# Optimization experiments

Hardware: AMD Instinct MI355X
Metric: run time of the kernel (lower is better)

Reference implementation:

```python
import jax, jax.numpy as jnp
import numpy as np

QMAX = 127.0  # int8 symmetric fake-quant (brevitas-style, per-tensor scale)

def fq(x):
    s = jnp.maximum(jnp.max(jnp.abs(x)), 1e-8) / QMAX
    q = jnp.clip(jnp.round(x / s), -QMAX - 1.0, QMAX) * s
    # straight-through estimator (round_ste), matches brevitas gradient behavior
    return x + jax.lax.stop_gradient(q - x)

def layernorm(x, g, b, eps=1e-5):
    m = x.mean(-1, keepdims=True)
    v = x.var(-1, keepdims=True)
    return (x - m) * jax.lax.rsqrt(v + eps) * g + b

def mamba_dir(u, W_in, conv_w, conv_b, W_xp, W_dt, b_dt, A_log, D_skip, W_out):
    # u: [B, L, D]
    B, L, D = u.shape
    di, K = conv_w.shape
    ds = A_log.shape[-1]
    dtr = W_dt.shape[0]
    xz = u @ W_in                              # [B, L, 2*di]
    xc, z = jnp.split(xz, 2, axis=-1)
    xb = xc.transpose(0, 2, 1)                 # [B, di, L]
    xb = jax.lax.conv_general_dilated(
        xb, conv_w[:, None, :], (1,), [(K - 1, 0)],
        feature_group_count=di,
        dimension_numbers=('NCH', 'OIH', 'NCH')) + conv_b[None, :, None]
    xs = jax.nn.silu(xb.transpose(0, 2, 1))    # [B, L, di]
    proj = xs @ W_xp                           # [B, L, dtr+2*ds]
    dt_in = proj[..., :dtr]
    Bc = proj[..., dtr:dtr + ds]
    Cc = proj[..., dtr + ds:]
    dt = jax.nn.softplus(dt_in @ W_dt + b_dt)  # [B, L, di]
    A = -jnp.exp(A_log)                        # [di, ds]

    def step(h, inp):
        dt_t, B_t, C_t, x_t = inp              # [B,di],[B,ds],[B,ds],[B,di]
        dA = jnp.exp(dt_t[..., None] * A)      # [B, di, ds]
        h = dA * h + (dt_t * x_t)[..., None] * B_t[:, None, :]
        y = jnp.einsum('bds,bs->bd', h, C_t)
        return h, y

    h0 = jnp.zeros((B, di, ds), u.dtype)
    t = lambda a: jnp.moveaxis(a, 1, 0)        # [L, B, ...]
    _, ys = jax.lax.scan(step, h0, (t(dt), t(Bc), t(Cc), t(xs)))
    y = jnp.moveaxis(ys, 0, 1) + xs * D_skip   # [B, L, di]
    y = y * jax.nn.silu(z)
    return y @ W_out                           # [B, L, D]


def setup_inputs() -> dict:
    key = jax.random.key(0)
    ks = jax.random.split(key, 20)
    B, H, W = 32, 16, 4096
    p = 2
    emb = 32
    gh, gw = (H - p) // p + 1, (W - p) // p + 1   # 8, 2048
    D = gh * emb                                   # 256
    di = min(2 * D, 256)                           # 256
    ds, K, nb, nc = 8, 4, 2, 10
    dtr = (D + 15) // 16                           # 16
    f32 = jnp.float32
    n = lambda k, s, sc: jax.random.normal(k, s, f32) * sc
    return {
        'x': jax.random.normal(ks[0], (B, 1, H, W), f32),
        'patch_w': n(ks[1], (emb, 1, p, p), 0.3),
        'patch_b': jnp.zeros((emb,), f32),
        'pos_embed': n(ks[2], (1, gw, D), 0.02),
        'W_in': n(ks[3], (nb, 2, D, 2 * di), D ** -0.5),
        'conv_w': n(ks[4], (nb, 2, di, K), 0.3),
        'conv_b': jnp.zeros((nb, 2, di), f32),
        'W_xp': n(ks[5], (nb, 2, di, dtr + 2 * ds), di ** -0.5),
        'W_dt': n(ks[6], (nb, 2, dtr, di), dtr ** -0.5),
        'b_dt': jnp.full((nb, 2, di), -3.0, f32),
        'A_log': jnp.log(jnp.broadcast_to(jnp.arange(1, ds + 1, dtype=f32), (nb, 2, di, ds))),
        'D_skip': jnp.ones((nb, 2, di), f32),
        'W_out': n(ks[7], (nb, 2, di, D), di ** -0.5),
        'ln_g': jnp.ones((nb, D), f32),
        'ln_b': jnp.zeros((nb, D), f32),
        'cls_w': n(ks[8], (nc, D), D ** -0.5),
        'cls_b': jnp.zeros((nc,), f32),
    }


def reference(x, patch_w, patch_b, pos_embed, W_in, conv_w, conv_b, W_xp, W_dt,
              b_dt, A_log, D_skip, W_out, ln_g, ln_b, cls_w, cls_b):
    x = fq(x)
    # quantized patch embed: conv2d stride=patch, then [B,C,gh,gw] -> [B, gw, gh*C]
    xe = jax.lax.conv_general_dilated(
        x, fq(patch_w), (2, 2), 'VALID',
        dimension_numbers=('NCHW', 'OIHW', 'NCHW')) + patch_b[None, :, None, None]
    B, C, gh, gw = xe.shape
    h = fq(xe.transpose(0, 3, 2, 1).reshape(B, gw, gh * C))
    pos = fq(pos_embed)
    h, pos = fq(h), fq(pos)     # scale_equalizer on both operands
    h = fq(h + pos)
    nb = W_in.shape[0]
    for i in range(nb):
        res = h
        yf = mamba_dir(h, W_in[i, 0], conv_w[i, 0], conv_b[i, 0], W_xp[i, 0],
                       W_dt[i, 0], b_dt[i, 0], A_log[i, 0], D_skip[i, 0], W_out[i, 0])
        yb = jnp.flip(mamba_dir(jnp.flip(h, 1), W_in[i, 1], conv_w[i, 1], conv_b[i, 1],
                                W_xp[i, 1], W_dt[i, 1], b_dt[i, 1], A_log[i, 1],
                                D_skip[i, 1], W_out[i, 1]), 1)
        y = fq(yf + yb)          # bidirectional_strategy='add' + block output quant
        h = fq(layernorm(res + y, ln_g[i], ln_b[i]))
    pooled = fq(h.mean(axis=1))  # AdaptiveAvgPool1d(1) over sequence
    return pooled @ fq(cls_w).T + cls_b
```

## Files before the change

kernel.cpp:

```cpp
#include <hip/hip_runtime.h>


typedef __attribute__((ext_vector_type(8))) short bfrag;
typedef __attribute__((ext_vector_type(4))) float cfrag;

__device__ __forceinline__ float fq_val(float x, float s){
  float q = rintf(x / s);
  q = fminf(fmaxf(q, -128.0f), 127.0f);
  return q * s;
}
__device__ __forceinline__ float g_of(float a){ return fmaxf(a, 1e-8f) / 127.0f; }

__device__ __forceinline__ short f2bf(float f){
  unsigned u = __float_as_uint(f);
  u += 0x7fff + ((u >> 16) & 1);
  return (short)(u >> 16);
}
__device__ __forceinline__ float bf2f(short h){
  return __uint_as_float(((unsigned)(unsigned short)h) << 16);
}

__device__ __forceinline__ void bk_absmax(float v, float* bkt){
  for (int m = 32; m; m >>= 1) v = fmaxf(v, __shfl_xor(v, m));
  __shared__ float wmax[4];
  int lane = threadIdx.x & 63, wid = threadIdx.x >> 6;
  if (lane == 0) wmax[wid] = v;
  __syncthreads();
  if (threadIdx.x == 0){
    float m = fmaxf(fmaxf(wmax[0], wmax[1]), fmaxf(wmax[2], wmax[3]));
    atomicMax((unsigned int*)&bkt[(blockIdx.x & 63) * 16], __float_as_uint(m));
  }
}

__global__ __launch_bounds__(256) void absmax_b(const float* __restrict__ x,
                                                long long n, float* __restrict__ bkt){
  float m = 0.0f;
  for (long long i = (long long)blockIdx.x * 256 + threadIdx.x; i < n;
       i += (long long)gridDim.x * 256)
    m = fmaxf(m, fabsf(x[i]));
  bk_absmax(m, bkt);
}

__global__ __launch_bounds__(64) void combine_kernel(const float* __restrict__ bkt,
                                                     float* __restrict__ slot){
  float v = bkt[(threadIdx.x & 63) * 16];
  for (int m = 32; m; m >>= 1) v = fmaxf(v, __shfl_xor(v, m));
  if (threadIdx.x == 0) slot[0] = v;
}

__global__ __launch_bounds__(64) void chain_kernel(float* __restrict__ sc){
  if (threadIdx.x == 0){
    float s1 = g_of(sc[1]);
    float a1 = fq_val(sc[1], s1);
    sc[2] = s1; sc[3] = g_of(a1);
    float p1 = g_of(sc[4]);
    float a2 = fq_val(sc[4], p1);
    sc[5] = p1; sc[6] = g_of(a2);
  }
}

__global__ __launch_bounds__(256) void fq_small(const float* __restrict__ src,
                                                float* __restrict__ dst, int n){
  __shared__ float red[256];
  __shared__ float sS;
  float m = 0.0f;
  for (int i = threadIdx.x; i < n; i += 256) m = fmaxf(m, fabsf(src[i]));
  red[threadIdx.x] = m; __syncthreads();
  for (int s2 = 128; s2 > 0; s2 >>= 1){
    if (threadIdx.x < s2) red[threadIdx.x] = fmaxf(red[threadIdx.x], red[threadIdx.x + s2]);
    __syncthreads();
  }
  if (threadIdx.x == 0) sS = g_of(red[0]);
  __syncthreads();
  float s = sS;
  for (int i = threadIdx.x; i < n; i += 256) dst[i] = fq_val(src[i], s);
}

__global__ __launch_bounds__(256) void wsplit(const float* __restrict__ src,
                                              short* __restrict__ dh,
                                              short* __restrict__ dl, int N){
  __shared__ float tile[64][65];
  int n0 = blockIdx.x * 64, k0 = blockIdx.y * 64, id = blockIdx.z;
  const float* S = src + (long long)id * 256 * N;
  short* H = dh + (long long)id * N * 256;
  short* L = dl + (long long)id * N * 256;
  int t = threadIdx.x;
#pragma unroll
  for (int i = 0; i < 16; i++){
    int idx = i * 256 + t;
    int kr = idx >> 6, nc = idx & 63;
    tile[kr][nc] = S[(long long)(k0 + kr) * N + n0 + nc];
  }
  __syncthreads();
#pragma unroll
  for (int i = 0; i < 16; i++){
    int idx = i * 256 + t;
    int nr = idx >> 6, kc = idx & 63;
    float f = tile[kc][nr];
    short h = f2bf(f);
    short l = f2bf(f - bf2f(h));
    H[(long long)(n0 + nr) * 256 + k0 + kc] = h;
    L[(long long)(n0 + nr) * 256 + k0 + kc] = l;
  }
}

__global__ __launch_bounds__(256) void patchify_kernel(const float* __restrict__ x,
                                                       const float* __restrict__ pwq,
                                                       const float* __restrict__ pb,
                                                       float* __restrict__ h,
                                                       const float* __restrict__ slot,
                                                       float* __restrict__ bkt){
  int t = blockIdx.x * 256 + threadIdx.x;
  int q = t & 63;
  int l = (t >> 6) & 2047;
  int b = t >> 17;
  int d0 = q * 4;
  int c0 = d0 & 31, g = d0 >> 5;
  float s = g_of(slot[0]);
  const float* xp = x + ((long long)(b * 16 + 2 * g) * 4096 + 2 * l);
  float x0 = fq_val(xp[0], s),    x1 = fq_val(xp[1], s);
  float x2 = fq_val(xp[4096], s), x3 = fq_val(xp[4097], s);
  float4 o; float* op = (float*)&o;
  float mx = 0.0f;
#pragma unroll
  for (int j = 0; j < 4; j++){
    int c = c0 + j;
    float a = pb[c] + x0 * pwq[c * 4] + x1 * pwq[c * 4 + 1]
                    + x2 * pwq[c * 4 + 2] + x3 * pwq[c * 4 + 3];
    op[j] = a; mx = fmaxf(mx, fabsf(a));
  }
  *(float4*)(h + (long long)t * 4) = o;
  bk_absmax(mx, bkt);
}

__global__ __launch_bounds__(256) void addpos_kernel(float* __restrict__ h,
                                                     const float* __restrict__ pos,
                                                     const float* __restrict__ sc,
                                                     float* __restrict__ bkt){
  long long t = (long long)blockIdx.x * 256 + threadIdx.x;
  float s1 = sc[2], s2 = sc[3], p1 = sc[5], p2 = sc[6];
  float4 hv = *(const float4*)(h + t * 4);
  float4 pv = *(const float4*)(pos + ((t * 4) & 524287));
  float* hp = (float*)&hv; float* pp = (float*)&pv;
  float4 o; float* op = (float*)&o;
  float mx = 0.0f;
#pragma unroll
  for (int j = 0; j < 4; j++){
    float v = fq_val(fq_val(hp[j], s1), s2) + fq_val(fq_val(pp[j], p1), p2);
    op[j] = v; mx = fmaxf(mx, fabsf(v));
  }
  *(float4*)(h + t * 4) = o;
  bk_absmax(mx, bkt);
}

__global__ __launch_bounds__(256) void aprep(const float* __restrict__ h,
                                             const float* __restrict__ slot,
                                             short* __restrict__ Aq){
  long long t = (long long)blockIdx.x * 256 + threadIdx.x;
  float sA = g_of(slot[0]);
  float4 v0 = *(const float4*)(h + t * 8);
  float4 v1 = *(const float4*)(h + t * 8 + 4);
  float* vp0 = (float*)&v0; float* vp1 = (float*)&v1;
  bfrag o;
#pragma unroll
  for (int j = 0; j < 4; j++){
    o[j]     = f2bf(fminf(fmaxf(rintf(vp0[j] / sA), -128.0f), 127.0f));
    o[j + 4] = f2bf(fminf(fmaxf(rintf(vp1[j] / sA), -128.0f), 127.0f));
  }
  *(bfrag*)(Aq + t * 8) = o;
}

__global__ __launch_bounds__(256) void gemm_win(const short* __restrict__ Aq,
                                                const short* __restrict__ BhT,
                                                const short* __restrict__ BlT,
                                                float* __restrict__ Cx,
                                                float* __restrict__ Cz,
                                                int flipA,
                                                const float* __restrict__ aslot){
  __shared__ short Ah[128][40];
  __shared__ short Bh[128][40];
  __shared__ short Bl[128][40];
  int t = threadIdx.x;
  int bn = blockIdx.x, bm = blockIdx.y;
  int lane = t & 63, wv = t >> 6;
  int wm = wv & 1, wn = wv >> 1;
  int qd = lane >> 4, l16 = lane & 15;
  float sA = g_of(aslot[0]);

  int r0s = t >> 2, c8s = (t & 3) * 8;
  int r1s = r0s + 64;
  long long am0, am1;
  {
    long long mg0 = (long long)bm * 128 + r0s;
    long long mg1 = (long long)bm * 128 + r1s;
    am0 = flipA ? ((mg0 & ~2047LL) + (2047 - (mg0 & 2047))) : mg0;
    am1 = flipA ? ((mg1 & ~2047LL) + (2047 - (mg1 & 2047))) : mg1;
  }
  const short* Aq0 = Aq + am0 * 256 + c8s;
  const short* Aq1 = Aq + am1 * 256 + c8s;
  const short* Bh0 = BhT + (long long)(bn * 128 + r0s) * 256 + c8s;
  const short* Bh1 = BhT + (long long)(bn * 128 + r1s) * 256 + c8s;
  const short* Bl0 = BlT + (long long)(bn * 128 + r0s) * 256 + c8s;
  const short* Bl1 = BlT + (long long)(bn * 128 + r1s) * 256 + c8s;

  bfrag aR0, aR1, bhR0, bhR1, blR0, blR1;
  aR0 = *(const bfrag*)(Aq0);   aR1 = *(const bfrag*)(Aq1);
  bhR0 = *(const bfrag*)(Bh0);  bhR1 = *(const bfrag*)(Bh1);
  blR0 = *(const bfrag*)(Bl0);  blR1 = *(const bfrag*)(Bl1);

  cfrag acc[4][4];
#pragma unroll
  for (int i = 0; i < 4; i++)
#pragma unroll
    for (int j = 0; j < 4; j++)
      acc[i][j] = (cfrag){0.f, 0.f, 0.f, 0.f};

  for (int k0 = 0; k0 < 256; k0 += 32){
    *(bfrag*)&Ah[r0s][c8s] = aR0;  *(bfrag*)&Ah[r1s][c8s] = aR1;
    *(bfrag*)&Bh[r0s][c8s] = bhR0; *(bfrag*)&Bh[r1s][c8s] = bhR1;
    *(bfrag*)&Bl[r0s][c8s] = blR0; *(bfrag*)&Bl[r1s][c8s] = blR1;
    __syncthreads();
    if (k0 < 224){
      int kn = k0 + 32;
      aR0 = *(const bfrag*)(Aq0 + kn);   aR1 = *(const bfrag*)(Aq1 + kn);
      bhR0 = *(const bfrag*)(Bh0 + kn);  bhR1 = *(const bfrag*)(Bh1 + kn);
      blR0 = *(const bfrag*)(Bl0 + kn);  blR1 = *(const bfrag*)(Bl1 + kn);
    }
    bfrag bh[4], bl[4], a[4];
#pragma unroll
    for (int ni = 0; ni < 4; ni++){
      int nrow = wn * 64 + ni * 16 + l16;
      bh[ni] = *(const bfrag*)&Bh[nrow][qd * 8];
      bl[ni] = *(const bfrag*)&Bl[nrow][qd * 8];
    }
#pragma unroll
    for (int mi = 0; mi < 4; mi++)
      a[mi] = *(const bfrag*)&Ah[wm * 64 + mi * 16 + l16][qd * 8];
#pragma unroll
    for (int mi = 0; mi < 4; mi++)
#pragma unroll
      for (int ni = 0; ni < 4; ni++)
        acc[mi][ni] = __builtin_amdgcn_mfma_f32_16x16x32_bf16(a[mi], bh[ni], acc[mi][ni], 0, 0, 0);
#pragma unroll
    for (int mi = 0; mi < 4; mi++)
#pragma unroll
      for (int ni = 0; ni < 4; ni++)
        acc[mi][ni] = __builtin_amdgcn_mfma_f32_16x16x32_bf16(a[mi], bl[ni], acc[mi][ni], 0, 0, 0);
    __syncthreads();
  }

  float* Co = (bn < 2) ? Cx : Cz;
  int cb = (bn & 1) * 128;
#pragma unroll
  for (int mi = 0; mi < 4; mi++){
#pragma unroll
    for (int ni = 0; ni < 4; ni++){
      int colg = cb + wn * 64 + ni * 16 + l16;
#pragma unroll
      for (int r = 0; r < 4; r++){
        long long mg = (long long)bm * 128 + wm * 64 + mi * 16 + qd * 4 + r;
        Co[mg * 256 + colg] = acc[mi][ni][r] * sA;
      }
    }
  }
}

__global__ __launch_bounds__(256) void gemm_wout(const float* __restrict__ A,
                                                 const short* __restrict__ BhT,
                                                 const short* __restrict__ BlT,
                                                 float* __restrict__ C,
                                                 int flipC, int accum,
                                                 float* __restrict__ bkt){
  __shared__ short Ah[128][40];
  __shared__ short Al[128][40];
  __shared__ short Bh[128][40];
  __shared__ short Bl[128][40];
  int t = threadIdx.x;
  int bn = blockIdx.x, bm = blockIdx.y;
  int lane = t & 63, wv = t >> 6;
  int wm = wv & 1, wn = wv >> 1;
  int qd = lane >> 4, l16 = lane & 15;

  int ra0 = t >> 3, ca0 = (t & 7) * 4;
  const float* Ap0 = A + ((long long)bm * 128 + ra0) * 256 + ca0;
  const float* Ap1 = Ap0 + 32 * 256;
  const float* Ap2 = Ap0 + 64 * 256;
  const float* Ap3 = Ap0 + 96 * 256;
  int rb0 = t >> 2, cb8 = (t & 3) * 8;
  int rb1 = rb0 + 64;
  const short* Bh0 = BhT + (long long)(bn * 128 + rb0) * 256 + cb8;
  const short* Bh1 = BhT + (long long)(bn * 128 + rb1) * 256 + cb8;
  const short* Bl0 = BlT + (long long)(bn * 128 + rb0) * 256 + cb8;
  const short* Bl1 = BlT + (long long)(bn * 128 + rb1) * 256 + cb8;

  uint4 aw0, aw1, aw2, aw3;
  bfrag bhR0, bhR1, blR0, blR1;
  aw0 = *(const uint4*)(Ap0); aw1 = *(const uint4*)(Ap1);
  aw2 = *(const uint4*)(Ap2); aw3 = *(const uint4*)(Ap3);
  bhR0 = *(const bfrag*)(Bh0); bhR1 = *(const bfrag*)(Bh1);
  blR0 = *(const bfrag*)(Bl0); blR1 = *(const bfrag*)(Bl1);

  cfrag acc[4][4];
#pragma unroll
  for (int i = 0; i < 4; i++)
#pragma unroll
    for (int j = 0; j < 4; j++)
      acc[i][j] = (cfrag){0.f, 0.f, 0.f, 0.f};

  for (int k0 = 0; k0 < 256; k0 += 32){
    {
      unsigned* w;
      w = (unsigned*)&aw0;
#pragma unroll
      for (int j = 0; j < 4; j++){ Ah[ra0][ca0+j] = (short)(w[j] & 0xffff); Al[ra0][ca0+j] = (short)(w[j] >> 16); }
      w = (unsigned*)&aw1;
#pragma unroll
      for (int j = 0; j < 4; j++){ Ah[ra0+32][ca0+j] = (short)(w[j] & 0xffff); Al[ra0+32][ca0+j] = (short)(w[j] >> 16); }
      w = (unsigned*)&aw2;
#pragma unroll
      for (int j = 0; j < 4; j++){ Ah[ra0+64][ca0+j] = (short)(w[j] & 0xffff); Al[ra0+64][ca0+j] = (short)(w[j] >> 16); }
      w = (unsigned*)&aw3;
#pragma unroll
      for (int j = 0; j < 4; j++){ Ah[ra0+96][ca0+j] = (short)(w[j] & 0xffff); Al[ra0+96][ca0+j] = (short)(w[j] >> 16); }
      *(bfrag*)&Bh[rb0][cb8] = bhR0; *(bfrag*)&Bh[rb1][cb8] = bhR1;
      *(bfrag*)&Bl[rb0][cb8] = blR0; *(bfrag*)&Bl[rb1][cb8] = blR1;
    }
    __syncthreads();
    if (k0 < 224){
      int kn = k0 + 32;
      aw0 = *(const uint4*)(Ap0 + kn); aw1 = *(const uint4*)(Ap1 + kn);
      aw2 = *(const uint4*)(Ap2 + kn); aw3 = *(const uint4*)(Ap3 + kn);
      bhR0 = *(const bfrag*)(Bh0 + kn); bhR1 = *(const bfrag*)(Bh1 + kn);
      blR0 = *(const bfrag*)(Bl0 + kn); blR1 = *(const bfrag*)(Bl1 + kn);
    }
    bfrag bh[4], bl[4], ah[4], al[4];
#pragma unroll
    for (int ni = 0; ni < 4; ni++){
      int nrow = wn * 64 + ni * 16 + l16;
      bh[ni] = *(const bfrag*)&Bh[nrow][qd * 8];
      bl[ni] = *(const bfrag*)&Bl[nrow][qd * 8];
    }
#pragma unroll
    for (int mi = 0; mi < 4; mi++){
      int mrow = wm * 64 + mi * 16 + l16;
      ah[mi] = *(const bfrag*)&Ah[mrow][qd * 8];
      al[mi] = *(const bfrag*)&Al[mrow][qd * 8];
    }
#pragma unroll
    for (int mi = 0; mi < 4; mi++)
#pragma unroll
      for (int ni = 0; ni < 4; ni++)
        acc[mi][ni] = __builtin_amdgcn_mfma_f32_16x16x32_bf16(ah[mi], bh[ni], acc[mi][ni], 0, 0, 0);
#pragma unroll
    for (int mi = 0; mi < 4; mi++)
#pragma unroll
      for (int ni = 0; ni < 4; ni++)
        acc[mi][ni] = __builtin_amdgcn_mfma_f32_16x16x32_bf16(al[mi], bh[ni], acc[mi][ni], 0, 0, 0);
#pragma unroll
    for (int mi = 0; mi < 4; mi++)
#pragma unroll
      for (int ni = 0; ni < 4; ni++)
        acc[mi][ni] = __builtin_amdgcn_mfma_f32_16x16x32_bf16(ah[mi], bl[ni], acc[mi][ni], 0, 0, 0);
    __syncthreads();
  }

  float mx = 0.0f;
#pragma unroll
  for (int mi = 0; mi < 4; mi++){
#pragma unroll
    for (int ni = 0; ni < 4; ni++){
      int colg = bn * 128 + wn * 64 + ni * 16 + l16;
#pragma unroll
      for (int r = 0; r < 4; r++){
        long long mg = (long long)bm * 128 + wm * 64 + mi * 16 + qd * 4 + r;
        long long mr = flipC ? ((mg & ~2047LL) + (2047 - (mg & 2047))) : mg;
        float* Cp = C + mr * 256 + colg;
        if (accum){
          float nv = *Cp + acc[mi][ni][r];
          *Cp = nv;
          mx = fmaxf(mx, fabsf(nv));
        } else {
          *Cp = acc[mi][ni][r];
        }
      }
    }
  }
  if (bkt) bk_absmax(mx, bkt);
}

__global__ __launch_bounds__(256) void conv_proj(const float* __restrict__ xc,
                                                 const float* __restrict__ cw,
                                                 const float* __restrict__ cb,
                                                 const float* __restrict__ Wxp,
                                                 float* __restrict__ xs,
                                                 float* __restrict__ proj){
  __shared__ float As[8][256];
  long long r0 = (long long)blockIdx.x * 8;
  int l0 = (int)(r0 & 2047);
  int d = threadIdx.x;
  float w0 = cw[d*4], w1 = cw[d*4+1], w2 = cw[d*4+2], w3 = cw[d*4+3];
  float cbd = cb[d];
  const float* base = xc + r0 * 256 + d;
  float vm3 = (l0 >= 3) ? base[-768] : 0.0f;
  float vm2 = (l0 >= 2) ? base[-512] : 0.0f;
  float vm1 = (l0 >= 1) ? base[-256] : 0.0f;
#pragma unroll
  for (int r = 0; r < 8; r++){
    float v0 = base[r * 256];
    float a = cbd + w3 * v0 + w2 * vm1 + w1 * vm2 + w0 * vm3;
    float sv = __fdividef(a, 1.0f + __expf(-a));
    As[r][d] = sv;
    xs[r0 * 256 + r * 256 + d] = sv;
    vm3 = vm2; vm2 = vm1; vm1 = v0;
  }
  __syncthreads();
  int rr = threadIdx.x >> 5, cc = threadIdx.x & 31;
  float acc = 0.0f;
#pragma unroll 8
  for (int k = 0; k < 256; k++) acc = fmaf(As[rr][k], Wxp[k * 32 + cc], acc);
  proj[(r0 + rr) * 32 + cc] = acc;
}

__global__ __launch_bounds__(256) void scan1_kernel(const float* __restrict__ xs,
                                                    const float* __restrict__ proj,
                                                    const float* __restrict__ Wdt,
                                                    const float* __restrict__ bdt,
                                                    const float* __restrict__ A_log,
                                                    float* __restrict__ Pb,
                                                    float* __restrict__ Qb){
  __shared__ float pj[32][32];
  int blk = blockIdx.x;
  int seg = blk & 63, b = blk >> 6;
  int d = threadIdx.x;
  long long rowbase = (long long)b * 2048 + seg * 32;
  {
    const float4* src4 = (const float4*)(proj + rowbase * 32);
    float4* dst4 = (float4*)&pj[0][0];
    if (threadIdx.x < 256) dst4[threadIdx.x] = src4[threadIdx.x];
  }
  __syncthreads();
  float wdt[16];
#pragma unroll
  for (int r = 0; r < 16; r++) wdt[r] = Wdt[r * 256 + d];
  float bd = bdt[d];
  float A[8];
#pragma unroll
  for (int s = 0; s < 8; s++) A[s] = -expf(A_log[d * 8 + s]);
  const float* xp = xs + rowbase * 256 + d;
  float P[8], q[8];
#pragma unroll
  for (int s = 0; s < 8; s++){ P[s] = 1.0f; q[s] = 0.0f; }
  for (int l = 0; l < 32; l++){
    float acc = bd;
#pragma unroll
    for (int r = 0; r < 16; r++) acc = fmaf(pj[l][r], wdt[r], acc);
    float e = __expf(-fabsf(acc));
    float dt = fmaxf(acc, 0.0f) + __logf(1.0f + e);
    float x = xp[(long long)l * 256];
    float dx = dt * x;
#pragma unroll
    for (int s = 0; s < 8; s++){
      float dA = __expf(dt * A[s]);
      P[s] *= dA;
      q[s] = fmaf(dA, q[s], dx * pj[l][16 + s]);
    }
  }
  long long obase = ((long long)blk << 11) + (long long)d * 8;
  *(float4*)(Pb + obase)     = make_float4(P[0], P[1], P[2], P[3]);
  *(float4*)(Pb + obase + 4) = make_float4(P[4], P[5], P[6], P[7]);
  *(float4*)(Qb + obase)     = make_float4(q[0], q[1], q[2], q[3]);
  *(float4*)(Qb + obase + 4) = make_float4(q[4], q[5], q[6], q[7]);
}

__global__ __launch_bounds__(256) void scan2_kernel(float* __restrict__ Pb,
                                                    const float* __restrict__ Qb){
  int t = blockIdx.x * 256 + threadIdx.x;
  int ds_ = t & 2047;
  int b = t >> 11;
  float h = 0.0f;
#pragma unroll
  for (int g = 0; g < 64; g++){
    long long idx = (((long long)b * 64 + g) << 11) + ds_;
    float tp = Pb[idx];
    Pb[idx] = h;
    h = fmaf(tp, h, Qb[idx]);
  }
}

__global__ __launch_bounds__(256) void scan3_kernel(const float* __restrict__ z,
                                                    float* __restrict__ xs,
                                                    const float* __restrict__ proj,
                                                    const float* __restrict__ Wdt,
                                                    const float* __restrict__ bdt,
                                                    const float* __restrict__ A_log,
                                                    const float* __restrict__ Dsk,
                                                    const float* __restrict__ Hs){
  __shared__ float pj[32][32];
  int blk = blockIdx.x;
  int seg = blk & 63, b = blk >> 6;
  int d = threadIdx.x;
  long long rowbase = (long long)b * 2048 + seg * 32;
  {
    const float4* src4 = (const float4*)(proj + rowbase * 32);
    float4* dst4 = (float4*)&pj[0][0];
    if (threadIdx.x < 256) dst4[threadIdx.x] = src4[threadIdx.x];
  }
  __syncthreads();
  float wdt[16];
#pragma unroll
  for (int r = 0; r < 16; r++) wdt[r] = Wdt[r * 256 + d];
  float bd = bdt[d];
  float A[8];
#pragma unroll
  for (int s = 0; s < 8; s++) A[s] = -expf(A_log[d * 8 + s]);
  float Dv = Dsk[d];
  long long hbase = ((long long)blk << 11) + (long long)d * 8;
  float4 h0 = *(const float4*)(Hs + hbase);
  float4 h1 = *(const float4*)(Hs + hbase + 4);
  float h[8] = {h0.x, h0.y, h0.z, h0.w, h1.x, h1.y, h1.z, h1.w};
  float* xp = xs + rowbase * 256 + d;
  const float* zp = z + rowbase * 256 + d;
  for (int l = 0; l < 32; l++){
    float acc = bd;
#pragma unroll
    for (int r = 0; r < 16; r++) acc = fmaf(pj[l][r], wdt[r], acc);
    float e = __expf(-fabsf(acc));
    float dt = fmaxf(acc, 0.0f) + __logf(1.0f + e);
    float x = xp[(long long)l * 256];
    float dx = dt * x;
    float y = 0.0f;
#pragma unroll
    for (int s = 0; s < 8; s++){
      float dA = __expf(dt * A[s]);
      h[s] = fmaf(dA, h[s], dx * pj[l][16 + s]);
      y = fmaf(h[s], pj[l][24 + s], y);
    }
    y = fmaf(x, Dv, y);
    float zv = zp[(long long)l * 256];
    float yg = y * __fdividef(zv, 1.0f + __expf(-zv));
    short hh = f2bf(yg);
    short ll = f2bf(yg - bf2f(hh));
    xp[(long long)l * 256] =
        __uint_as_float(((unsigned)(unsigned short)ll << 16) | (unsigned short)hh);
  }
}

__global__ __launch_bounds__(256) void ln_kernel(const float* __restrict__ hraw,
                                                 const float* __restrict__ hslot,
                                                 float* __restrict__ y,
                                                 const float* __restrict__ yslot,
                                                 const float* __restrict__ g,
                                                 const float* __restrict__ bb,
                                                 float* __restrict__ bkt){
  int wid = threadIdx.x >> 6, lane = threadIdx.x & 63;
  long long row = (long long)blockIdx.x * 4 + wid;
  long long o = row * 256 + lane * 4;
  float sh = g_of(hslot[0]);
  float sy = g_of(yslot[0]);
  float4 hv = *(const float4*)(hraw + o);
  float4 yv = *(const float4*)(y + o);
  float t0 = fq_val(hv.x, sh) + fq_val(yv.x, sy);
  float t1 = fq_val(hv.y, sh) + fq_val(yv.y, sy);
  float t2 = fq_val(hv.z, sh) + fq_val(yv.z, sy);
  float t3 = fq_val(hv.w, sh) + fq_val(yv.w, sy);
  float sum = t0 + t1 + t2 + t3;
  for (int m = 32; m; m >>= 1) sum += __shfl_xor(sum, m);
  float mean = sum * (1.0f / 256.0f);
  float d0 = t0 - mean, d1 = t1 - mean, d2 = t2 - mean, d3 = t3 - mean;
  float vs = d0 * d0 + d1 * d1 + d2 * d2 + d3 * d3;
  for (int m = 32; m; m >>= 1) vs += __shfl_xor(vs, m);
  float r = rsqrtf(vs * (1.0f / 256.0f) + 1e-5f);
  float4 gv = *(const float4*)(g + lane * 4);
  float4 bv = *(const float4*)(bb + lane * 4);
  float4 ov;
  ov.x = d0 * r * gv.x + bv.x;
  ov.y = d1 * r * gv.y + bv.y;
  ov.z = d2 * r * gv.z + bv.z;
  ov.w = d3 * r * gv.w + bv.w;
  *(float4*)(y + o) = ov;
  float mx = fmaxf(fmaxf(fabsf(ov.x), fabsf(ov.y)), fmaxf(fabsf(ov.z), fabsf(ov.w)));
  bk_absmax(mx, bkt);
}

__global__ __launch_bounds__(256) void mean_part(const float* __restrict__ h,
                                                 const float* __restrict__ slot,
                                                 float* __restrict__ part){
  int blk = blockIdx.x;
  int d = threadIdx.x;
  int lc = blk & 63, b = blk >> 6;
  float s = g_of(slot[0]);
  const float* p = h + ((long long)b * 2048 + lc * 32) * 256 + d;
  float a = 0.0f;
  for (int l = 0; l < 32; l++) a += fq_val(p[(long long)l * 256], s);
  part[(long long)blk * 256 + d] = a;
}

__global__ __launch_bounds__(256) void mean_fin(const float* __restrict__ part,
                                                float* __restrict__ pooled){
  int idx = blockIdx.x * 256 + threadIdx.x;
  int d = idx & 255, b = idx >> 8;
  float a = 0.0f;
  for (int lc = 0; lc < 64; lc++)
    a += part[((long long)b * 64 + lc) * 256 + d];
  pooled[idx] = a * (1.0f / 2048.0f);
}

__global__ __launch_bounds__(320) void cls_kernel(const float* __restrict__ pooled,
                                                  const float* __restrict__ clsq,
                                                  const float* __restrict__ cb,
                                                  float* __restrict__ out){
  int tid = threadIdx.x;
  if (tid >= 320) return;
  int b = tid / 10, n = tid - b * 10;
  float acc = cb[n];
  const float* pr = pooled + b * 256;
  const float* wr = clsq + n * 256;
  for (int dd = 0; dd < 256; dd++) acc = fmaf(pr[dd], wr[dd], acc);
  out[tid] = acc;
}

extern "C" void kernel_launch(void* const* d_in, const int* in_sizes, int n_in,
                              void* d_out, int out_size, void* d_ws, size_t ws_size,
                              hipStream_t stream) {
  const float* x_in   = (const float*)d_in[0];
  const float* pw_in  = (const float*)d_in[1];
  const float* pb_in  = (const float*)d_in[2];
  const float* pos_in = (const float*)d_in[3];
  const float* Win    = (const float*)d_in[4];
  const float* convw  = (const float*)d_in[5];
  const float* convb  = (const float*)d_in[6];
  const float* Wxp    = (const float*)d_in[7];
  const float* Wdt    = (const float*)d_in[8];
  const float* bdt    = (const float*)d_in[9];
  const float* Alog   = (const float*)d_in[10];
  const float* Dsk    = (const float*)d_in[11];
  const float* Wout   = (const float*)d_in[12];
  const float* lng    = (const float*)d_in[13];
  const float* lnb    = (const float*)d_in[14];
  const float* clsw   = (const float*)d_in[15];
  const float* clsb   = (const float*)d_in[16];
  float* out = (float*)d_out;

  float* W = (float*)d_ws;
  float* sc     = W;
  float* bkt    = W + 64;
  float* pwq    = W + 8256;
  float* clsq   = W + 8384;
  float* pooled = W + 10944;
  float* wsplit_base = W + 19136;
  short* winHs  = (short*)wsplit_base;
  short* winLs  = winHs + 524288;
  short* woutHs = winLs + 524288;
  short* woutLs = woutHs + 262144;
  float* hbuf   = wsplit_base + 786432;
  float* ybuf   = hbuf + 16777216;
  float* chunkW = ybuf + 16777216;
  float* mpart  = chunkW;

  const size_t fixed_f  = 34360000ULL;
  const size_t perseq_f = 2162688ULL;
  long long avail = (long long)(ws_size / 4) - (long long)fixed_f;
  int CB = (int)(avail / (long long)perseq_f);
  if (CB > 32) CB = 32;
  if (CB < 1) CB = 1;

  hipMemsetAsync(sc, 0, (64 + 8 * 1024) * sizeof(float), stream);

  wsplit<<<dim3(8, 4, 4), 256, 0, stream>>>(Win, winHs, winLs, 512);
  wsplit<<<dim3(4, 4, 4), 256, 0, stream>>>(Wout, woutHs, woutLs, 256);

  absmax_b<<<2048, 256, 0, stream>>>(x_in, 2097152LL, bkt + 0 * 1024);
  combine_kernel<<<1, 64, 0, stream>>>(bkt + 0 * 1024, sc + 0);
  fq_small<<<1, 256, 0, stream>>>(pw_in, pwq, 128);
  patchify_kernel<<<16384, 256, 0, stream>>>(x_in, pwq, pb_in, hbuf, sc + 0,
                                             bkt + 1 * 1024);
  combine_kernel<<<1, 64, 0, stream>>>(bkt + 1 * 1024, sc + 1);
  absmax_b<<<1024, 256, 0, stream>>>(pos_in, 524288LL, bkt + 2 * 1024);
  combine_kernel<<<1, 64, 0, stream>>>(bkt + 2 * 1024, sc + 4);
  chain_kernel<<<1, 64, 0, stream>>>(sc);
  addpos_kernel<<<16384, 256, 0, stream>>>(hbuf, pos_in, sc, bkt + 3 * 1024);
  combine_kernel<<<1, 64, 0, stream>>>(bkt + 3 * 1024, sc + 7);

  for (int i = 0; i < 2; i++){
    float* hin = (i == 0) ? hbuf : ybuf;
    float* yac = (i == 0) ? ybuf : hbuf;
    float* hs  = sc + (i == 0 ? 7 : 9);
    float* ys  = sc + (i == 0 ? 8 : 10);
    float* ybk = bkt + (i == 0 ? 4 : 6) * 1024;
    float* hbk = bkt + (i == 0 ? 5 : 7) * 1024;
    for (int b0 = 0; b0 < 32; ){
      int rows = (32 - b0 < CB) ? (32 - b0) : CB;
      long long R = (long long)rows * 2048;
      short* Aq_c   = (short*)chunkW;
      float* xc_c   = chunkW + R * 128;
      float* z_c    = xc_c + R * 256;
      float* xs_c   = z_c + R * 256;
      float* proj_c = xs_c + R * 256;
      float* Pb_c   = proj_c + R * 32;
      float* Qb_c   = Pb_c + (long long)rows * 131072;
      const float* hA = hin + (long long)b0 * 524288;
      float*       yC = yac + (long long)b0 * 524288;

      aprep<<<rows * 256, 256, 0, stream>>>(hA, hs, Aq_c);

      for (int dir = 0; dir < 2; dir++){
        int idx = i * 2 + dir;
        gemm_win<<<dim3(4, R / 128), 256, 0, stream>>>(
            Aq_c, winHs + (long long)idx * 131072, winLs + (long long)idx * 131072,
            xc_c, z_c, dir, hs);
        conv_proj<<<R / 8, 256, 0, stream>>>(xc_c, convw + idx * 1024,
                                             convb + idx * 256, Wxp + idx * 8192,
                                             xs_c, proj_c);
        scan1_kernel<<<rows * 64, 256, 0, stream>>>(xs_c, proj_c,
                                                    Wdt + idx * 4096, bdt + idx * 256,
                                                    Alog + idx * 2048, Pb_c, Qb_c);
        scan2_kernel<<<rows * 8, 256, 0, stream>>>(Pb_c, Qb_c);
        scan3_kernel<<<rows * 64, 256, 0, stream>>>(z_c, xs_c, proj_c,
                                                    Wdt + idx * 4096, bdt + idx * 256,
                                                    Alog + idx * 2048,
                                                    Dsk + idx * 256, Pb_c);
        gemm_wout<<<dim3(2, R / 128), 256, 0, stream>>>(
            xs_c, woutHs + (long long)idx * 65536, woutLs + (long long)idx * 65536,
            yC, dir, dir, dir ? ybk : nullptr);
      }
      b0 += rows;
    }
    combine_kernel<<<1, 64, 0, stream>>>(ybk, ys);
    ln_kernel<<<16384, 256, 0, stream>>>(hin, hs, yac, ys, lng + i * 256,
                                         lnb + i * 256, hbk);
    combine_kernel<<<1, 64, 0, stream>>>(hbk, sc + (i == 0 ? 9 : 11));
  }
  mean_part<<<2048, 256, 0, stream>>>(hbuf, sc + 11, mpart);
  mean_fin<<<32, 256, 0, stream>>>(mpart, pooled);
  fq_small<<<1, 256, 0, stream>>>(pooled, pooled, 8192);
  fq_small<<<1, 256, 0, stream>>>(clsw, clsq, 2560);
  cls_kernel<<<1, 320, 0, stream>>>(pooled, clsq, clsb, out);
}
```

Measured before the change: 1.825 ms.

## Fuse conv+proj into scan pass 1, recompute conv in scan3, shrink GEMM M-tile

Merges the depthwise causal conv, SiLU and x_proj GEMV into the first scan kernel so xs never round-trips through global memory before the scan. The third scan kernel recomputes the conv+SiLU from xc instead of reading xs, and still writes gated output into xs for the out-projection. The in- and out-projection GEMMs drop from 128-row to 64-row M tiles, doubling block count and halving accumulator registers per wave at the cost of re-reading the B tiles more often. Duplicated conv arithmetic and a larger 32KB shared tile in cps1 are the trade-offs.

```diff
diff --git a/kernel.cpp b/kernel.cpp
--- a/kernel.cpp
+++ b/kernel.cpp
@@ -177,88 +177,81 @@
                                                 float* __restrict__ Cz,
                                                 int flipA,
                                                 const float* __restrict__ aslot){
-  __shared__ short Ah[128][40];
+  __shared__ short Ah[64][40];
   __shared__ short Bh[128][40];
   __shared__ short Bl[128][40];
   int t = threadIdx.x;
   int bn = blockIdx.x, bm = blockIdx.y;
   int lane = t & 63, wv = t >> 6;
-  int wm = wv & 1, wn = wv >> 1;
   int qd = lane >> 4, l16 = lane & 15;
   float sA = g_of(aslot[0]);
 
-  int r0s = t >> 2, c8s = (t & 3) * 8;
-  int r1s = r0s + 64;
-  long long am0, am1;
-  {
-    long long mg0 = (long long)bm * 128 + r0s;
-    long long mg1 = (long long)bm * 128 + r1s;
-    am0 = flipA ? ((mg0 & ~2047LL) + (2047 - (mg0 & 2047))) : mg0;
-    am1 = flipA ? ((mg1 & ~2047LL) + (2047 - (mg1 & 2047))) : mg1;
-  }
-  const short* Aq0 = Aq + am0 * 256 + c8s;
-  const short* Aq1 = Aq + am1 * 256 + c8s;
-  const short* Bh0 = BhT + (long long)(bn * 128 + r0s) * 256 + c8s;
-  const short* Bh1 = BhT + (long long)(bn * 128 + r1s) * 256 + c8s;
-  const short* Bl0 = BlT + (long long)(bn * 128 + r0s) * 256 + c8s;
-  const short* Bl1 = BlT + (long long)(bn * 128 + r1s) * 256 + c8s;
-
-  bfrag aR0, aR1, bhR0, bhR1, blR0, blR1;
-  aR0 = *(const bfrag*)(Aq0);   aR1 = *(const bfrag*)(Aq1);
-  bhR0 = *(const bfrag*)(Bh0);  bhR1 = *(const bfrag*)(Bh1);
-  blR0 = *(const bfrag*)(Bl0);  blR1 = *(const bfrag*)(Bl1);
-
-  cfrag acc[4][4];
+  int ar = t >> 2, c8s = (t & 3) * 8;
+  long long mgA = (long long)bm * 64 + ar;
+  long long amr = flipA ? ((mgA & ~2047LL) + (2047 - (mgA & 2047))) : mgA;
+  const short* Aq0 = Aq + amr * 256 + c8s;
+  int br0 = ar, br1 = ar + 64;
+  const short* Bh0 = BhT + (long long)(bn * 128 + br0) * 256 + c8s;
+  const short* Bh1 = BhT + (long long)(bn * 128 + br1) * 256 + c8s;
+  const short* Bl0 = BlT + (long long)(bn * 128 + br0) * 256 + c8s;
+  const short* Bl1 = BlT + (long long)(bn * 128 + br1) * 256 + c8s;
+
+  bfrag aR, bhR0, bhR1, blR0, blR1;
+  aR = *(const bfrag*)(Aq0);
+  bhR0 = *(const bfrag*)(Bh0); bhR1 = *(const bfrag*)(Bh1);
+  blR0 = *(const bfrag*)(Bl0); blR1 = *(const bfrag*)(Bl1);
+
+  cfrag acc[4][2];
 #pragma unroll
   for (int i = 0; i < 4; i++)
 #pragma unroll
-    for (int j = 0; j < 4; j++)
+    for (int j = 0; j < 2; j++)
       acc[i][j] = (cfrag){0.f, 0.f, 0.f, 0.f};
 
   for (int k0 = 0; k0 < 256; k0 += 32){
-    *(bfrag*)&Ah[r0s][c8s] = aR0;  *(bfrag*)&Ah[r1s][c8s] = aR1;
-    *(bfrag*)&Bh[r0s][c8s] = bhR0; *(bfrag*)&Bh[r1s][c8s] = bhR1;
-    *(bfrag*)&Bl[r0s][c8s] = blR0; *(bfrag*)&Bl[r1s][c8s] = blR1;
+    *(bfrag*)&Ah[ar][c8s] = aR;
+    *(bfrag*)&Bh[br0][c8s] = bhR0; *(bfrag*)&Bh[br1][c8s] = bhR1;
+    *(bfrag*)&Bl[br0][c8s] = blR0; *(bfrag*)&Bl[br1][c8s] = blR1;
     __syncthreads();
     if (k0 < 224){
       int kn = k0 + 32;
-      aR0 = *(const bfrag*)(Aq0 + kn);   aR1 = *(const bfrag*)(Aq1 + kn);
-      bhR0 = *(const bfrag*)(Bh0 + kn);  bhR1 = *(const bfrag*)(Bh1 + kn);
-      blR0 = *(const bfrag*)(Bl0 + kn);  blR1 = *(const bfrag*)(Bl1 + kn);
-    }
-    bfrag bh[4], bl[4], a[4];
-#pragma unroll
-    for (int ni = 0; ni < 4; ni++){
-      int nrow = wn * 64 + ni * 16 + l16;
+      aR = *(const bfrag*)(Aq0 + kn);
+      bhR0 = *(const bfrag*)(Bh0 + kn); bhR1 = *(const bfrag*)(Bh1 + kn);
+      blR0 = *(const bfrag*)(Bl0 + kn); blR1 = *(const bfrag*)(Bl1 + kn);
+    }
+    bfrag a[4], bh[2], bl[2];
+#pragma unroll
+    for (int ni = 0; ni < 2; ni++){
+      int nrow = wv * 32 + ni * 16 + l16;
       bh[ni] = *(const bfrag*)&Bh[nrow][qd * 8];
       bl[ni] = *(const bfrag*)&Bl[nrow][qd * 8];
     }
 #pragma unroll
     for (int mi = 0; mi < 4; mi++)
-      a[mi] = *(const bfrag*)&Ah[wm * 64 + mi * 16 + l16][qd * 8];
+      a[mi] = *(const bfrag*)&Ah[mi * 16 + l16][qd * 8];
 #pragma unroll
     for (int mi = 0; mi < 4; mi++)
 #pragma unroll
-      for (int ni = 0; ni < 4; ni++)
+      for (int ni = 0; ni < 2; ni++)
         acc[mi][ni] = __builtin_amdgcn_mfma_f32_16x16x32_bf16(a[mi], bh[ni], acc[mi][ni], 0, 0, 0);
 #pragma unroll
     for (int mi = 0; mi < 4; mi++)
 #pragma unroll
-      for (int ni = 0; ni < 4; ni++)
+      for (int ni = 0; ni < 2; ni++)
         acc[mi][ni] = __builtin_amdgcn_mfma_f32_16x16x32_bf16(a[mi], bl[ni], acc[mi][ni], 0, 0, 0);
     __syncthreads();
   }
 
   float* Co = (bn < 2) ? Cx : Cz;
-  int cb = (bn & 1) * 128;
+  int cbase = (bn & 1) * 128;
 #pragma unroll
   for (int mi = 0; mi < 4; mi++){
 #pragma unroll
-    for (int ni = 0; ni < 4; ni++){
-      int colg = cb + wn * 64 + ni * 16 + l16;
+    for (int ni = 0; ni < 2; ni++){
+      int colg = cbase + wv * 32 + ni * 16 + l16;
 #pragma unroll
       for (int r = 0; r < 4; r++){
-        long long mg = (long long)bm * 128 + wm * 64 + mi * 16 + qd * 4 + r;
+        long long mg = (long long)bm * 64 + mi * 16 + qd * 4 + r;
         Co[mg * 256 + colg] = acc[mi][ni][r] * sA;
       }
     }
@@ -271,95 +264,83 @@
                                                  float* __restrict__ C,
                                                  int flipC, int accum,
                                                  float* __restrict__ bkt){
-  __shared__ short Ah[128][40];
-  __shared__ short Al[128][40];
+  __shared__ short Ah[64][40];
+  __shared__ short Al[64][40];
   __shared__ short Bh[128][40];
   __shared__ short Bl[128][40];
   int t = threadIdx.x;
   int bn = blockIdx.x, bm = blockIdx.y;
   int lane = t & 63, wv = t >> 6;
-  int wm = wv & 1, wn = wv >> 1;
   int qd = lane >> 4, l16 = lane & 15;
 
-  int ra0 = t >> 3, ca0 = (t & 7) * 4;
-  const float* Ap0 = A + ((long long)bm * 128 + ra0) * 256 + ca0;
+  int ra = t >> 3, ca = (t & 7) * 4;
+  const float* Ap0 = A + ((long long)bm * 64 + ra) * 256 + ca;
   const float* Ap1 = Ap0 + 32 * 256;
-  const float* Ap2 = Ap0 + 64 * 256;
-  const float* Ap3 = Ap0 + 96 * 256;
-  int rb0 = t >> 2, cb8 = (t & 3) * 8;
-  int rb1 = rb0 + 64;
-  const short* Bh0 = BhT + (long long)(bn * 128 + rb0) * 256 + cb8;
-  const short* Bh1 = BhT + (long long)(bn * 128 + rb1) * 256 + cb8;
-  const short* Bl0 = BlT + (long long)(bn * 128 + rb0) * 256 + cb8;
-  const short* Bl1 = BlT + (long long)(bn * 128 + rb1) * 256 + cb8;
-
-  uint4 aw0, aw1, aw2, aw3;
+  int br0 = t >> 2, c8s = (t & 3) * 8;
+  int br1 = br0 + 64;
+  const short* Bh0 = BhT + (long long)(bn * 128 + br0) * 256 + c8s;
+  const short* Bh1 = BhT + (long long)(bn * 128 + br1) * 256 + c8s;
+  const short* Bl0 = BlT + (long long)(bn * 128 + br0) * 256 + c8s;
+  const short* Bl1 = BlT + (long long)(bn * 128 + br1) * 256 + c8s;
+
+  uint4 aw0, aw1;
   bfrag bhR0, bhR1, blR0, blR1;
   aw0 = *(const uint4*)(Ap0); aw1 = *(const uint4*)(Ap1);
-  aw2 = *(const uint4*)(Ap2); aw3 = *(const uint4*)(Ap3);
   bhR0 = *(const bfrag*)(Bh0); bhR1 = *(const bfrag*)(Bh1);
   blR0 = *(const bfrag*)(Bl0); blR1 = *(const bfrag*)(Bl1);
 
-  cfrag acc[4][4];
+  cfrag acc[4][2];
 #pragma unroll
   for (int i = 0; i < 4; i++)
 #pragma unroll
-    for (int j = 0; j < 4; j++)
+    for (int j = 0; j < 2; j++)
       acc[i][j] = (cfrag){0.f, 0.f, 0.f, 0.f};
 
   for (int k0 = 0; k0 < 256; k0 += 32){
     {
-      unsigned* w;
-      w = (unsigned*)&aw0;
-#pragma unroll
-      for (int j = 0; j < 4; j++){ Ah[ra0][ca0+j] = (short)(w[j] & 0xffff); Al[ra0][ca0+j] = (short)(w[j] >> 16); }
+      unsigned* w = (unsigned*)&aw0;
+#pragma unroll
+      for (int j = 0; j < 4; j++){ Ah[ra][ca+j] = (short)(w[j] & 0xffff); Al[ra][ca+j] = (short)(w[j] >> 16); }
       w = (unsigned*)&aw1;
 #pragma unroll
-      for (int j = 0; j < 4; j++){ Ah[ra0+32][ca0+j] = (short)(w[j] & 0xffff); Al[ra0+32][ca0+j] = (short)(w[j] >> 16); }
-      w = (unsigned*)&aw2;
-#pragma unroll
-      for (int j = 0; j < 4; j++){ Ah[ra0+64][ca0+j] = (short)(w[j] & 0xffff); Al[ra0+64][ca0+j] = (short)(w[j] >> 16); }
-      w = (unsigned*)&aw3;
-#pragma unroll
-      for (int j = 0; j < 4; j++){ Ah[ra0+96][ca0+j] = (short)(w[j] & 0xffff); Al[ra0+96][ca0+j] = (short)(w[j] >> 16); }
-      *(bfrag*)&Bh[rb0][cb8] = bhR0; *(bfrag*)&Bh[rb1][cb8] = bhR1;
-      *(bfrag*)&Bl[rb0][cb8] = blR0; *(bfrag*)&Bl[rb1][cb8] = blR1;
+      for (int j = 0; j < 4; j++){ Ah[ra+32][ca+j] = (short)(w[j] & 0xffff); Al[ra+32][ca+j] = (short)(w[j] >> 16); }
+      *(bfrag*)&Bh[br0][c8s] = bhR0; *(bfrag*)&Bh[br1][c8s] = bhR1;
+      *(bfrag*)&Bl[br0][c8s] = blR0; *(bfrag*)&Bl[br1][c8s] = blR1;
     }
     __syncthreads();
     if (k0 < 224){
       int kn = k0 + 32;
       aw0 = *(const uint4*)(Ap0 + kn); aw1 = *(const uint4*)(Ap1 + kn);
-      aw2 = *(const uint4*)(Ap2 + kn); aw3 = *(const uint4*)(Ap3 + kn);
       bhR0 = *(const bfrag*)(Bh0 + kn); bhR1 = *(const bfrag*)(Bh1 + kn);
       blR0 = *(const bfrag*)(Bl0 + kn); blR1 = *(const bfrag*)(Bl1 + kn);
     }
-    bfrag bh[4], bl[4], ah[4], al[4];
-#pragma unroll
-    for (int ni = 0; ni < 4; ni++){
-      int nrow = wn * 64 + ni * 16 + l16;
+    bfrag bh[2], bl[2], ah[4], al[4];
+#pragma unroll
+    for (int ni = 0; ni < 2; ni++){
+      int nrow = wv * 32 + ni * 16 + l16;
       bh[ni] = *(const bfrag*)&Bh[nrow][qd * 8];
       bl[ni] = *(const bfrag*)&Bl[nrow][qd * 8];
     }
 #pragma unroll
     for (int mi = 0; mi < 4; mi++){
-      int mrow = wm * 64 + mi * 16 + l16;
+      int mrow = mi * 16 + l16;
       ah[mi] = *(const bfrag*)&Ah[mrow][qd * 8];
       al[mi] = *(const bfrag*)&Al[mrow][qd * 8];
     }
 #pragma unroll
     for (int mi = 0; mi < 4; mi++)
 #pragma unroll
-      for (int ni = 0; ni < 4; ni++)
+      for (int ni = 0; ni < 2; ni++)
         acc[mi][ni] = __builtin_amdgcn_mfma_f32_16x16x32_bf16(ah[mi], bh[ni], acc[mi][ni], 0, 0, 0);
 #pragma unroll
     for (int mi = 0; mi < 4; mi++)
 #pragma unroll
-      for (int ni = 0; ni < 4; ni++)
+      for (int ni = 0; ni < 2; ni++)
         acc[mi][ni] = __builtin_amdgcn_mfma_f32_16x16x32_bf16(al[mi], bh[ni], acc[mi][ni], 0, 0, 0);
 #pragma unroll
     for (int mi = 0; mi < 4; mi++)
 #pragma unroll
-      for (int ni = 0; ni < 4; ni++)
+      for (int ni = 0; ni < 2; ni++)
         acc[mi][ni] = __builtin_amdgcn_mfma_f32_16x16x32_bf16(ah[mi], bl[ni], acc[mi][ni], 0, 0, 0);
     __syncthreads();
   }
@@ -368,11 +349,11 @@
 #pragma unroll
   for (int mi = 0; mi < 4; mi++){
 #pragma unroll
-    for (int ni = 0; ni < 4; ni++){
-      int colg = bn * 128 + wn * 64 + ni * 16 + l16;
+    for (int ni = 0; ni < 2; ni++){
+      int colg = bn * 128 + wv * 32 + ni * 16 + l16;
 #pragma unroll
       for (int r = 0; r < 4; r++){
-        long long mg = (long long)bm * 128 + wm * 64 + mi * 16 + qd * 4 + r;
+        long long mg = (long long)bm * 64 + mi * 16 + qd * 4 + r;
         long long mr = flipC ? ((mg & ~2047LL) + (2047 - (mg & 2047))) : mg;
         float* Cp = C + mr * 256 + colg;
         if (accum){
@@ -388,55 +369,51 @@
   if (bkt) bk_absmax(mx, bkt);
 }
 
-__global__ __launch_bounds__(256) void conv_proj(const float* __restrict__ xc,
-                                                 const float* __restrict__ cw,
-                                                 const float* __restrict__ cb,
-                                                 const float* __restrict__ Wxp,
-                                                 float* __restrict__ xs,
-                                                 float* __restrict__ proj){
-  __shared__ float As[8][256];
-  long long r0 = (long long)blockIdx.x * 8;
-  int l0 = (int)(r0 & 2047);
-  int d = threadIdx.x;
-  float w0 = cw[d*4], w1 = cw[d*4+1], w2 = cw[d*4+2], w3 = cw[d*4+3];
-  float cbd = cb[d];
-  const float* base = xc + r0 * 256 + d;
-  float vm3 = (l0 >= 3) ? base[-768] : 0.0f;
-  float vm2 = (l0 >= 2) ? base[-512] : 0.0f;
-  float vm1 = (l0 >= 1) ? base[-256] : 0.0f;
-#pragma unroll
-  for (int r = 0; r < 8; r++){
-    float v0 = base[r * 256];
-    float a = cbd + w3 * v0 + w2 * vm1 + w1 * vm2 + w0 * vm3;
-    float sv = __fdividef(a, 1.0f + __expf(-a));
-    As[r][d] = sv;
-    xs[r0 * 256 + r * 256 + d] = sv;
-    vm3 = vm2; vm2 = vm1; vm1 = v0;
-  }
-  __syncthreads();
-  int rr = threadIdx.x >> 5, cc = threadIdx.x & 31;
-  float acc = 0.0f;
-#pragma unroll 8
-  for (int k = 0; k < 256; k++) acc = fmaf(As[rr][k], Wxp[k * 32 + cc], acc);
-  proj[(r0 + rr) * 32 + cc] = acc;
-}
-
-__global__ __launch_bounds__(256) void scan1_kernel(const float* __restrict__ xs,
-                                                    const float* __restrict__ proj,
-                                                    const float* __restrict__ Wdt,
-                                                    const float* __restrict__ bdt,
-                                                    const float* __restrict__ A_log,
-                                                    float* __restrict__ Pb,
-                                                    float* __restrict__ Qb){
+__global__ __launch_bounds__(256) void cps1_kernel(const float* __restrict__ xc,
+                                                   const float* __restrict__ cw,
+                                                   const float* __restrict__ cb,
+                                                   const float* __restrict__ Wxp,
+                                                   float* __restrict__ proj,
+                                                   const float* __restrict__ Wdt,
+                                                   const float* __restrict__ bdt,
+                                                   const float* __restrict__ A_log,
+                                                   float* __restrict__ Pb,
+                                                   float* __restrict__ Qb){
+  __shared__ float As[32][256];
   __shared__ float pj[32][32];
   int blk = blockIdx.x;
   int seg = blk & 63, b = blk >> 6;
   int d = threadIdx.x;
   long long rowbase = (long long)b * 2048 + seg * 32;
+  int l0 = seg * 32;
+
   {
-    const float4* src4 = (const float4*)(proj + rowbase * 32);
-    float4* dst4 = (float4*)&pj[0][0];
-    if (threadIdx.x < 256) dst4[threadIdx.x] = src4[threadIdx.x];
+    float w0 = cw[d*4], w1 = cw[d*4+1], w2 = cw[d*4+2], w3 = cw[d*4+3];
+    float cbd = cb[d];
+    const float* base = xc + rowbase * 256 + d;
+    float vm3 = (l0 >= 3) ? base[-768] : 0.0f;
+    float vm2 = (l0 >= 2) ? base[-512] : 0.0f;
+    float vm1 = (l0 >= 1) ? base[-256] : 0.0f;
+#pragma unroll 4
+    for (int l = 0; l < 32; l++){
+      float v0 = base[(long long)l * 256];
+      float a = cbd + w3 * v0 + w2 * vm1 + w1 * vm2 + w0 * vm3;
+      As[l][d] = __fdividef(a, 1.0f + __expf(-a));
+      vm3 = vm2; vm2 = vm1; vm1 = v0;
+    }
+  }
+  __syncthreads();
+  {
+    int rr = d >> 5, cc = d & 31;
+#pragma unroll
+    for (int j = 0; j < 4; j++){
+      int row = rr + 8 * j;
+      float acc = 0.0f;
+#pragma unroll 8
+      for (int k = 0; k < 256; k++) acc = fmaf(As[row][k], Wxp[k * 32 + cc], acc);
+      pj[row][cc] = acc;
+      proj[(rowbase + row) * 32 + cc] = acc;
+    }
   }
   __syncthreads();
   float wdt[16];
@@ -446,7 +423,6 @@
   float A[8];
 #pragma unroll
   for (int s = 0; s < 8; s++) A[s] = -expf(A_log[d * 8 + s]);
-  const float* xp = xs + rowbase * 256 + d;
   float P[8], q[8];
 #pragma unroll
   for (int s = 0; s < 8; s++){ P[s] = 1.0f; q[s] = 0.0f; }
@@ -456,7 +432,7 @@
     for (int r = 0; r < 16; r++) acc = fmaf(pj[l][r], wdt[r], acc);
     float e = __expf(-fabsf(acc));
     float dt = fmaxf(acc, 0.0f) + __logf(1.0f + e);
-    float x = xp[(long long)l * 256];
+    float x = As[l][d];
     float dx = dt * x;
 #pragma unroll
     for (int s = 0; s < 8; s++){
@@ -487,9 +463,12 @@
   }
 }
 
-__global__ __launch_bounds__(256) void scan3_kernel(const float* __restrict__ z,
+__global__ __launch_bounds__(256) void scan3_kernel(const float* __restrict__ xc,
+                                                    const float* __restrict__ z,
                                                     float* __restrict__ xs,
                                                     const float* __restrict__ proj,
+                                                    const float* __restrict__ cw,
+                                                    const float* __restrict__ cb,
                                                     const float* __restrict__ Wdt,
                                                     const float* __restrict__ bdt,
                                                     const float* __restrict__ A_log,
@@ -500,6 +479,7 @@
   int seg = blk & 63, b = blk >> 6;
   int d = threadIdx.x;
   long long rowbase = (long long)b * 2048 + seg * 32;
+  int l0 = seg * 32;
   {
     const float4* src4 = (const float4*)(proj + rowbase * 32);
     float4* dst4 = (float4*)&pj[0][0];
@@ -514,19 +494,28 @@
 #pragma unroll
   for (int s = 0; s < 8; s++) A[s] = -expf(A_log[d * 8 + s]);
   float Dv = Dsk[d];
+  float w0 = cw[d*4], w1 = cw[d*4+1], w2 = cw[d*4+2], w3 = cw[d*4+3];
+  float cbd = cb[d];
   long long hbase = ((long long)blk << 11) + (long long)d * 8;
   float4 h0 = *(const float4*)(Hs + hbase);
   float4 h1 = *(const float4*)(Hs + hbase + 4);
   float h[8] = {h0.x, h0.y, h0.z, h0.w, h1.x, h1.y, h1.z, h1.w};
+  const float* base = xc + rowbase * 256 + d;
+  float vm3 = (l0 >= 3) ? base[-768] : 0.0f;
+  float vm2 = (l0 >= 2) ? base[-512] : 0.0f;
+  float vm1 = (l0 >= 1) ? base[-256] : 0.0f;
   float* xp = xs + rowbase * 256 + d;
   const float* zp = z + rowbase * 256 + d;
   for (int l = 0; l < 32; l++){
+    float v0 = base[(long long)l * 256];
+    float a0 = cbd + w3 * v0 + w2 * vm1 + w1 * vm2 + w0 * vm3;
+    float x = __fdividef(a0, 1.0f + __expf(-a0));
+    vm3 = vm2; vm2 = vm1; vm1 = v0;
     float acc = bd;
 #pragma unroll
     for (int r = 0; r < 16; r++) acc = fmaf(pj[l][r], wdt[r], acc);
     float e = __expf(-fabsf(acc));
     float dt = fmaxf(acc, 0.0f) + __logf(1.0f + e);
-    float x = xp[(long long)l * 256];
     float dx = dt * x;
     float y = 0.0f;
 #pragma unroll
@@ -705,21 +694,19 @@
 
       for (int dir = 0; dir < 2; dir++){
         int idx = i * 2 + dir;
-        gemm_win<<<dim3(4, R / 128), 256, 0, stream>>>(
+        gemm_win<<<dim3(4, R / 64), 256, 0, stream>>>(
             Aq_c, winHs + (long long)idx * 131072, winLs + (long long)idx * 131072,
             xc_c, z_c, dir, hs);
-        conv_proj<<<R / 8, 256, 0, stream>>>(xc_c, convw + idx * 1024,
-                                             convb + idx * 256, Wxp + idx * 8192,
-                                             xs_c, proj_c);
-        scan1_kernel<<<rows * 64, 256, 0, stream>>>(xs_c, proj_c,
-                                                    Wdt + idx * 4096, bdt + idx * 256,
-                                                    Alog + idx * 2048, Pb_c, Qb_c);
+        cps1_kernel<<<rows * 64, 256, 0, stream>>>(
+            xc_c, convw + idx * 1024, convb + idx * 256, Wxp + idx * 8192,
+            proj_c, Wdt + idx * 4096, bdt + idx * 256, Alog + idx * 2048,
+            Pb_c, Qb_c);
         scan2_kernel<<<rows * 8, 256, 0, stream>>>(Pb_c, Qb_c);
-        scan3_kernel<<<rows * 64, 256, 0, stream>>>(z_c, xs_c, proj_c,
-                                                    Wdt + idx * 4096, bdt + idx * 256,
-                                                    Alog + idx * 2048,
-                                                    Dsk + idx * 256, Pb_c);
-        gemm_wout<<<dim3(2, R / 128), 256, 0, stream>>>(
+        scan3_kernel<<<rows * 64, 256, 0, stream>>>(
+            xc_c, z_c, xs_c, proj_c, convw + idx * 1024, convb + idx * 256,
+            Wdt + idx * 4096, bdt + idx * 256, Alog + idx * 2048,
+            Dsk + idx * 256, Pb_c);
+        gemm_wout<<<dim3(2, R / 64), 256, 0, stream>>>(
             xs_c, woutHs + (long long)idx * 65536, woutLs + (long long)idx * 65536,
             yC, dir, dir, dir ? ybk : nullptr);
       }
```

Measured after the change: 1.944 ms. 6.5% more time.
